# Kernel optimization log

Measured on AMD Instinct MI355X. Metric: run time of the kernel, lower is better.

## Reference

```python
import jax, jax.numpy as jnp
import numpy as np

H1, H2, H3 = 32, 64, 64
NODEN = 12
NODES_PER_GRAPH = NODEN + 2  # 14
N = 700000                   # 50000 graphs * 14 nodes
E = 4000000


def setup_inputs() -> dict:
    key = jax.random.key(0)
    ks = jax.random.split(key, 8)
    x = jax.random.normal(ks[0], (N, H1), dtype=jnp.float32)
    edges = jax.random.randint(ks[1], (2, E), 0, N, dtype=jnp.int64)
    W1 = jax.random.normal(ks[2], (H1, H2), dtype=jnp.float32) / np.sqrt(H1).astype(np.float32)
    b1 = jnp.zeros((H2,), jnp.float32)
    W2 = jax.random.normal(ks[3], (H2, H3), dtype=jnp.float32) / np.sqrt(H2).astype(np.float32)
    b2 = jnp.zeros((H3,), jnp.float32)
    Wfc = jax.random.normal(ks[4], (H3 * NODES_PER_GRAPH, 1), dtype=jnp.float32) / np.sqrt(H3 * NODES_PER_GRAPH).astype(np.float32)
    bfc = jnp.zeros((1,), jnp.float32)
    return {"x": x, "edges": edges, "W1": W1, "b1": b1, "W2": W2, "b2": b2, "Wfc": Wfc, "bfc": bfc}


def gcn_conv(x, src, dst, W, b, n):
    # PyG GCNConv: h = X W; add self-loops; norm = deg^-1/2[src]*deg^-1/2[dst]
    h = x @ W  # [N, out]
    ones = jnp.ones(src.shape[0], dtype=h.dtype)
    deg = jax.ops.segment_sum(ones, dst, num_segments=n) + jnp.asarray(1.0, h.dtype)  # +1 self-loop
    dinv = jax.lax.rsqrt(deg)  # deg >= 1 always (self-loop)
    norm = dinv[src] * dinv[dst]  # [E]
    agg = jax.ops.segment_sum(h[src] * norm[:, None], dst, num_segments=n)
    agg = agg + h * (dinv * dinv)[:, None]  # self-loop contribution
    return agg + b


def reference(x, edges, W1, b1, W2, b2, Wfc, bfc):
    src, dst = edges[0], edges[1]
    h = jax.nn.relu(gcn_conv(x, src, dst, W1, b1, N))
    # F.dropout(training=False) is identity in eval mode
    h = jax.nn.relu(gcn_conv(h, src, dst, W2, b2, N))
    h = h.reshape(-1, H3 * NODES_PER_GRAPH)  # [B, 896]
    return h @ Wfc + bfc  # [B, 1]
```

## Files before the change

### kernel.cpp

```cpp
#include <hip/hip_runtime.h>
#include <hip/hip_fp16.h>


typedef _Float16 half8 __attribute__((ext_vector_type(8)));
typedef float float4v __attribute__((ext_vector_type(4)));

#define CHUNK 8192
#define BSH 11
#define BNODES 2048
#define DBINS 64

__global__ __launch_bounds__(256) void fallback_kernel(float* __restrict__ out, int n, float v)
{
  int i = blockIdx.x * 256 + threadIdx.x;
  if (i < n) out[i] = v;
}

__global__ __launch_bounds__(64) void probe_kernel(const int* __restrict__ edges, int* __restrict__ flag)
{
  if (threadIdx.x == 0) {
    int orv = edges[1] | edges[3] | edges[5] | edges[7] | edges[9] | edges[11] | edges[13] | edges[15];
    flag[0] = (orv == 0) ? 1 : 0;
  }
}

__global__ __launch_bounds__(64) void zero_dummy_kernel(
    __half* __restrict__ P, __half* __restrict__ F2, int* __restrict__ dhist, int N)
{
  int t = threadIdx.x;
  dhist[t] = 0;
  if (t < 8) ((uint2*)(P + (size_t)N * 32))[t] = make_uint2(0, 0);
  else if (t < 24) ((uint2*)(F2 + (size_t)N * 64))[t - 8] = make_uint2(0, 0);
}

__global__ __launch_bounds__(256) void hist2_kernel(
    const int* __restrict__ edges, int E, int N, const int* __restrict__ flag,
    int* __restrict__ cnt, int NBK)
{
  __shared__ int lh[512];
  int t = threadIdx.x;
  int blk = blockIdx.x;
  for (int b = t; b < NBK; b += 256) lh[b] = 0;
  __syncthreads();
  int sh = flag[0];
  int base = blk * CHUNK;
#pragma unroll
  for (int k = 0; k < CHUNK / 256; k++) {
    int e = base + k * 256 + t;
    if (e < E) {
      int d = edges[(E + e) << sh];
      if ((unsigned)d < (unsigned)N) atomicAdd(&lh[d >> BSH], 1);
    }
  }
  __syncthreads();
  for (int b = t; b < NBK; b += 256) cnt[(size_t)blk * NBK + b] = lh[b];
}

__global__ __launch_bounds__(64) void colscan_kernel(
    int* __restrict__ cnt, int NCH, int NBK, int* __restrict__ totals)
{
  int b = blockIdx.x;
  int lane = threadIdx.x;
  int carry = 0;
  int rounds = (NCH + 63) >> 6;
  for (int r = 0; r < rounds; r++) {
    int blk = r * 64 + lane;
    int v = (blk < NCH) ? cnt[(size_t)blk * NBK + b] : 0;
    int incl = v;
#pragma unroll
    for (int off = 1; off < 64; off <<= 1) {
      int x = __shfl_up(incl, off);
      if (lane >= off) incl += x;
    }
    int excl = incl - v + carry;
    if (blk < NCH) cnt[(size_t)blk * NBK + b] = excl;
    carry += __shfl(incl, 63);
  }
  if (lane == 0) totals[b] = carry;
}

__global__ __launch_bounds__(512) void scan_totals_kernel(
    const int* __restrict__ totals, int NBK,
    int* __restrict__ bstart, int* __restrict__ rowptr, int N)
{
  __shared__ int sm[512];
  int t = threadIdx.x;
  int v = (t < NBK) ? totals[t] : 0;
  sm[t] = v;
  __syncthreads();
  for (int off = 1; off < 512; off <<= 1) {
    int x = 0;
    if (t >= off) x = sm[t - off];
    __syncthreads();
    if (t >= off) sm[t] += x;
    __syncthreads();
  }
  if (t < NBK) bstart[t] = sm[t] - v;
  if (t == 0) { bstart[NBK] = sm[511]; rowptr[N] = sm[511] + N; }
}

__global__ __launch_bounds__(256) void pass3_kernel(
    const int* __restrict__ edges, int E, int N, const int* __restrict__ flag,
    const int* __restrict__ cnt, const int* __restrict__ bstart,
    int* __restrict__ pair, int NBK)
{
  __shared__ int lcur[512];
  int t = threadIdx.x;
  int blk = blockIdx.x;
  for (int b = t; b < NBK; b += 256)
    lcur[b] = bstart[b] + cnt[(size_t)blk * NBK + b];
  __syncthreads();
  int sh = flag[0];
  int base = blk * CHUNK;
#pragma unroll
  for (int k = 0; k < CHUNK / 256; k++) {
    int e = base + k * 256 + t;
    if (e < E) {
      int s = edges[e << sh];
      int d = edges[(E + e) << sh];
      if ((unsigned)s < (unsigned)N && (unsigned)d < (unsigned)N) {
        int pos = atomicAdd(&lcur[d >> BSH], 1);
        pair[pos] = s | ((d & (BNODES - 1)) << 20);
      }
    }
  }
}

__global__ __launch_bounds__(256) void build_kernel(
    const int* __restrict__ pair, const int* __restrict__ bstart,
    int* __restrict__ rowptr, float* __restrict__ dinv, int* __restrict__ col, int N)
{
  __shared__ int hist[BNODES];
  __shared__ int cur[BNODES];
  __shared__ int sc[256];
  int b = blockIdx.x;
  int t = threadIdx.x;
  int pbeg = bstart[b], pend = bstart[b + 1];
  int colbase = pbeg + (b << BSH);
#pragma unroll
  for (int i = 0; i < BNODES / 256; i++) {
    int idx = i * 256 + t;
    int row = (b << BSH) + idx;
    hist[idx] = (row < N) ? 1 : 0;
  }
  __syncthreads();
  for (int p = pbeg + t; p < pend; p += 256)
    atomicAdd(&hist[(pair[p] >> 20) & (BNODES - 1)], 1);
  __syncthreads();
  int hv[8];
  int tsum = 0;
#pragma unroll
  for (int i = 0; i < 8; i++) { hv[i] = hist[t * 8 + i]; tsum += hv[i]; }
  sc[t] = tsum;
  __syncthreads();
  for (int off = 1; off < 256; off <<= 1) {
    int x = 0;
    if (t >= off) x = sc[t - off];
    __syncthreads();
    if (t >= off) sc[t] += x;
    __syncthreads();
  }
  int run = sc[t] - tsum;
#pragma unroll
  for (int i = 0; i < 8; i++) {
    int idx = t * 8 + i;
    int rp = colbase + run;
    int row = (b << BSH) + idx;
    if (row < N) {
      rowptr[row] = rp;
      dinv[row] = rsqrtf((float)hv[i]);
      col[rp] = row;
      cur[idx] = rp + 1;
    } else {
      cur[idx] = rp;
    }
    run += hv[i];
  }
  __syncthreads();
  for (int p = pbeg + t; p < pend; p += 256) {
    int v = pair[p];
    int pos = atomicAdd(&cur[(v >> 20) & (BNODES - 1)], 1);
    col[pos] = v & 0xFFFFF;
  }
}

__global__ __launch_bounds__(256) void deg_hist_kernel(
    const int* __restrict__ rowptr, int* __restrict__ dhist, int N)
{
  __shared__ int lh[DBINS];
  int t = threadIdx.x;
  if (t < DBINS) lh[t] = 0;
  __syncthreads();
  int n = blockIdx.x * 256 + t;
  if (n < N) {
    int rlen = rowptr[n + 1] - rowptr[n];
    int b = rlen < DBINS ? rlen : DBINS - 1;
    atomicAdd(&lh[b], 1);
  }
  __syncthreads();
  if (t < DBINS && lh[t]) atomicAdd(&dhist[t], lh[t]);
}

__global__ __launch_bounds__(64) void deg_scan_kernel(
    const int* __restrict__ dhist, int* __restrict__ dcur)
{
  int t = threadIdx.x;
  int v = dhist[t];
  int incl = v;
#pragma unroll
  for (int off = 1; off < 64; off <<= 1) {
    int x = __shfl_up(incl, off);
    if (t >= off) incl += x;
  }
  dcur[t] = incl - v;
}

__global__ __launch_bounds__(256) void deg_place_kernel(
    const int* __restrict__ rowptr, const float* __restrict__ dinv, int* __restrict__ dcur,
    int* __restrict__ perm, int* __restrict__ iperm,
    int2* __restrict__ rowinfo, float* __restrict__ dinv_p, int N)
{
  __shared__ int lh[DBINS];
  __shared__ int lbase[DBINS];
  int t = threadIdx.x;
  if (t < DBINS) lh[t] = 0;
  __syncthreads();
  int n = blockIdx.x * 256 + t;
  int b = -1, rbeg = 0, rlen = 0;
  if (n < N) {
    rbeg = rowptr[n];
    rlen = rowptr[n + 1] - rbeg;
    b = rlen < DBINS ? rlen : DBINS - 1;
    atomicAdd(&lh[b], 1);
  }
  __syncthreads();
  if (t < DBINS) lbase[t] = lh[t] ? atomicAdd(&dcur[t], lh[t]) : 0;
  __syncthreads();
  if (t < DBINS) lh[t] = lbase[t];
  __syncthreads();
  if (n < N) {
    int pos = atomicAdd(&lh[b], 1);
    perm[pos] = n;
    iperm[n] = pos;
    rowinfo[pos] = make_int2(rbeg, rlen);
    dinv_p[pos] = dinv[n];
  }
}

__global__ __launch_bounds__(256) void remap_col_kernel(
    int* __restrict__ col, const int* __restrict__ iperm,
    const int* __restrict__ rowptr, int N)
{
  int total = rowptr[N];
  int stride = gridDim.x * 256;
  for (int k = blockIdx.x * 256 + threadIdx.x; k < total; k += stride)
    col[k] = iperm[col[k]];
}

__global__ __launch_bounds__(256) void scale_x_perm_kernel(
    const float* __restrict__ X, const int* __restrict__ perm,
    const float* __restrict__ dinv_p, __half* __restrict__ P, int N)
{
  int idx = blockIdx.x * 256 + threadIdx.x;
  int total = N * 4;
  int stride = gridDim.x * 256;
  for (int i = idx; i < total; i += stride) {
    int pos = i >> 2, part = i & 3;
    int node = perm[pos];
    const float4* xp = (const float4*)(X + (size_t)node * 32 + part * 8);
    float dv = dinv_p[pos];
    float4 v0 = xp[0], v1 = xp[1];
    half8 h;
    h[0] = (_Float16)(dv * v0.x); h[1] = (_Float16)(dv * v0.y);
    h[2] = (_Float16)(dv * v0.z); h[3] = (_Float16)(dv * v0.w);
    h[4] = (_Float16)(dv * v1.x); h[5] = (_Float16)(dv * v1.y);
    h[6] = (_Float16)(dv * v1.z); h[7] = (_Float16)(dv * v1.w);
    *(half8*)(P + (size_t)pos * 32 + part * 8) = h;
  }
}

__device__ inline void hacc(uint4 v, __half2* a)
{
  a[0] = __hadd2(a[0], *reinterpret_cast<__half2*>(&v.x));
  a[1] = __hadd2(a[1], *reinterpret_cast<__half2*>(&v.y));
  a[2] = __hadd2(a[2], *reinterpret_cast<__half2*>(&v.z));
  a[3] = __hadd2(a[3], *reinterpret_cast<__half2*>(&v.w));
}

__global__ __launch_bounds__(256) void agg1_pos_kernel(
    const __half* __restrict__ P, const int2* __restrict__ rowinfo,
    const int* __restrict__ col, const float* __restrict__ dinv_p,
    const float* __restrict__ W1, const float* __restrict__ b1,
    __half* __restrict__ U, int ntiles, int ndummy)
{
  int lane = threadIdx.x & 63;
  int n16 = lane & 15;
  int quad = lane >> 4;

  half8 bf[4];
#pragma unroll
  for (int jb = 0; jb < 4; jb++)
#pragma unroll
    for (int i = 0; i < 8; i++)
      bf[jb][i] = (_Float16)W1[(quad * 8 + i) * 64 + jb * 16 + n16];
  float b1j[4];
#pragma unroll
  for (int jb = 0; jb < 4; jb++) b1j[jb] = b1[jb * 16 + n16];

  const uint4* P4 = (const uint4*)P;
  _Float16* Uh = (_Float16*)U;
  int wave = (blockIdx.x * 256 + threadIdx.x) >> 6;
  int nw = (gridDim.x * 256) >> 6;
  for (int tile = wave; tile < ntiles; tile += nw) {
    int ut = __builtin_amdgcn_readfirstlane(tile);
    int base = ut * 16;
    int2 ri = rowinfo[base + n16];
    int rbeg = ri.x, rlen = ri.y;
    float dvown = dinv_p[base + n16];

    __half2 z2 = __float2half2_rn(0.f);
    __half2 aA[4] = {z2, z2, z2, z2};
    __half2 aB[4] = {z2, z2, z2, z2};

    for (int j = 0; __any(j < rlen); j += 8) {
      int c[8];
#pragma unroll
      for (int q = 0; q < 8; q++) {
        int cc = col[rbeg + j + q];
        c[q] = (j + q < rlen) ? cc : ndummy;
      }
      uint4 v[8];
#pragma unroll
      for (int q = 0; q < 8; q++) v[q] = P4[((size_t)c[q] << 2) + quad];
#pragma unroll
      for (int q = 0; q < 8; q += 2) { hacc(v[q], aA); hacc(v[q + 1], aB); }
    }
#pragma unroll
    for (int k = 0; k < 4; k++) aA[k] = __hadd2(aA[k], aB[k]);

    half8 a = *reinterpret_cast<half8*>(aA);
    float4v co[4];
#pragma unroll
    for (int jb = 0; jb < 4; jb++) {
      float4v z = {0.f, 0.f, 0.f, 0.f};
      co[jb] = __builtin_amdgcn_mfma_f32_16x16x32_f16(a, bf[jb], z, 0, 0, 0);
    }
#pragma unroll
    for (int r = 0; r < 4; r++) {
      int pos2 = base + quad * 4 + r;
      float dv = __shfl(dvown, quad * 4 + r);
#pragma unroll
      for (int jb = 0; jb < 4; jb++) {
        float h = dv * co[jb][r] + b1j[jb];
        h = h > 0.f ? h : 0.f;
        Uh[(size_t)pos2 * 64 + jb * 16 + n16] = (_Float16)(dv * h);
      }
    }
  }
}

__global__ __launch_bounds__(256) void out_init_kernel(
    float* __restrict__ out, const float* __restrict__ bfc, int n)
{
  int i = blockIdx.x * 256 + threadIdx.x;
  if (i < n) out[i] = bfc[0];
}

__global__ __launch_bounds__(256) void mfma_final_fused_kernel(
    const __half* __restrict__ U, const int2* __restrict__ rowinfo,
    const int* __restrict__ col, const float* __restrict__ dinv_p,
    const int* __restrict__ perm,
    const float* __restrict__ W2, const float* __restrict__ b2,
    const float* __restrict__ Wfc, float* __restrict__ out,
    int ntiles, int ndummy)
{
  int lane = threadIdx.x & 63;
  int n16 = lane & 15;
  int quad = lane >> 4;

  half8 bf[4][2];
#pragma unroll
  for (int jb = 0; jb < 4; jb++)
#pragma unroll
    for (int kf = 0; kf < 2; kf++)
#pragma unroll
      for (int i = 0; i < 8; i++)
        bf[jb][kf][i] = (_Float16)W2[(kf * 32 + quad * 8 + i) * 64 + jb * 16 + n16];
  float b2j[4];
#pragma unroll
  for (int jb = 0; jb < 4; jb++) b2j[jb] = b2[jb * 16 + n16];

  const uint4* U4 = (const uint4*)U;
  int wave = (blockIdx.x * 256 + threadIdx.x) >> 6;
  int nw = (gridDim.x * 256) >> 6;
  for (int tile = wave; tile < ntiles; tile += nw) {
    int ut = __builtin_amdgcn_readfirstlane(tile);
    int base = ut * 16;
    int2 ri = rowinfo[base + n16];
    int rbeg = ri.x, rlen = ri.y;
    int node = perm[base + n16];
    float dvown = dinv_p[base + n16];

    __half2 z2 = __float2half2_rn(0.f);
    __half2 aE0[4] = {z2, z2, z2, z2};
    __half2 aE1[4] = {z2, z2, z2, z2};
    __half2 aO0[4] = {z2, z2, z2, z2};
    __half2 aO1[4] = {z2, z2, z2, z2};

    for (int j = 0; __any(j < rlen); j += 4) {
      int c0 = col[rbeg + j];
      int c1 = col[rbeg + j + 1];
      int c2 = col[rbeg + j + 2];
      int c3 = col[rbeg + j + 3];
      c0 = (j < rlen) ? c0 : ndummy;
      c1 = (j + 1 < rlen) ? c1 : ndummy;
      c2 = (j + 2 < rlen) ? c2 : ndummy;
      c3 = (j + 3 < rlen) ? c3 : ndummy;
      uint4 v00 = U4[((size_t)c0 << 3) + quad];
      uint4 v01 = U4[((size_t)c0 << 3) + 4 + quad];
      uint4 v10 = U4[((size_t)c1 << 3) + quad];
      uint4 v11 = U4[((size_t)c1 << 3) + 4 + quad];
      uint4 v20 = U4[((size_t)c2 << 3) + quad];
      uint4 v21 = U4[((size_t)c2 << 3) + 4 + quad];
      uint4 v30 = U4[((size_t)c3 << 3) + quad];
      uint4 v31 = U4[((size_t)c3 << 3) + 4 + quad];
      hacc(v00, aE0); hacc(v01, aE1);
      hacc(v10, aO0); hacc(v11, aO1);
      hacc(v20, aE0); hacc(v21, aE1);
      hacc(v30, aO0); hacc(v31, aO1);
    }
#pragma unroll
    for (int k = 0; k < 4; k++) {
      aE0[k] = __hadd2(aE0[k], aO0[k]);
      aE1[k] = __hadd2(aE1[k], aO1[k]);
    }
    __half2 dv = __half2half2(__float2half_rn(dvown));
#pragma unroll
    for (int j = 0; j < 4; j++) {
      aE0[j] = __hmul2(aE0[j], dv);
      aE1[j] = __hmul2(aE1[j], dv);
    }
    half8 a0 = *reinterpret_cast<half8*>(aE0);
    half8 a1 = *reinterpret_cast<half8*>(aE1);

    int g_r[4], t_r[4];
#pragma unroll
    for (int r = 0; r < 4; r++) {
      int nd = __shfl(node, quad * 4 + r);
      g_r[r] = nd / 14;
      t_r[r] = nd - g_r[r] * 14;
    }
    float pr[4] = {0.f, 0.f, 0.f, 0.f};
#pragma unroll
    for (int jb = 0; jb < 4; jb++) {
      float4v acc = {0.f, 0.f, 0.f, 0.f};
      acc = __builtin_amdgcn_mfma_f32_16x16x32_f16(a0, bf[jb][0], acc, 0, 0, 0);
      acc = __builtin_amdgcn_mfma_f32_16x16x32_f16(a1, bf[jb][1], acc, 0, 0, 0);
      int j = jb * 16 + n16;
#pragma unroll
      for (int r = 0; r < 4; r++) {
        float h = acc[r] + b2j[jb];
        h = h > 0.f ? h : 0.f;
        pr[r] += h * Wfc[t_r[r] * 64 + j];
      }
    }
#pragma unroll
    for (int r = 0; r < 4; r++) {
#pragma unroll
      for (int off = 1; off < 16; off <<= 1) pr[r] += __shfl_xor(pr[r], off);
    }
    if (n16 == 0) {
#pragma unroll
      for (int r = 0; r < 4; r++) atomicAdd(&out[g_r[r]], pr[r]);
    }
  }
}

extern "C" void kernel_launch(void* const* d_in, const int* in_sizes, int n_in,
                              void* d_out, int out_size, void* d_ws, size_t ws_size,
                              hipStream_t stream)
{
  const float* x = (const float*)d_in[0];
  const int* edges = (const int*)d_in[1];
  const float* W1 = (const float*)d_in[2];
  const float* b1 = (const float*)d_in[3];
  const float* W2 = (const float*)d_in[4];
  const float* b2 = (const float*)d_in[5];
  const float* Wfc = (const float*)d_in[6];
  const float* bfc = (const float*)d_in[7];
  float* out = (float*)d_out;
  (void)n_in;

  const int N = in_sizes[0] / 32;
  const int E = in_sizes[1] / 2;
  const int B = out_size;
  const int NBK = (N + BNODES - 1) >> BSH;
  const int NCH = (E + CHUNK - 1) / CHUNK;
  const int NBLK = (N + 255) / 256;

  char* ws = (char*)d_ws;
  size_t off = 0;
  auto alloc = [&](size_t bytes) -> void* {
    void* p = ws + off;
    off += (bytes + 255) & ~(size_t)255;
    return p;
  };
  int* flag = (int*)alloc(256);
  int* cnt = (int*)alloc((size_t)NCH * NBK * 4);
  int* totals = (int*)alloc((size_t)NBK * 4);
  int* bstart = (int*)alloc(((size_t)NBK + 1) * 4);
  int* col = (int*)alloc(((size_t)E + N + 256) * 4);
  int* rowptr = (int*)alloc(((size_t)N + 1) * 4);
  float* dinv = (float*)alloc((size_t)N * 4);
  int* dhist = (int*)alloc(DBINS * 4);
  int* dcur = (int*)alloc(DBINS * 4);
  int* perm = (int*)alloc((size_t)N * 4);
  int* iperm = (int*)alloc((size_t)N * 4);
  int2* rowinfo = (int2*)alloc((size_t)N * 8);
  float* dinv_p = (float*)alloc((size_t)N * 4);
  __half* P = (__half*)alloc(((size_t)N + 16) * 32 * 2);
  __half* F2 = (__half*)alloc(((size_t)N + 16) * 64 * 2);
  int* pair = (int*)P;

  if (off > ws_size) {
    float v = -(float)(double)(ws_size >> 20);
    fallback_kernel<<<(B + 255) / 256, 256, 0, stream>>>(out, B, v);
    return;
  }

  probe_kernel<<<1, 64, 0, stream>>>(edges, flag);
  zero_dummy_kernel<<<1, 64, 0, stream>>>(P, F2, dhist, N);
  hist2_kernel<<<NCH, 256, 0, stream>>>(edges, E, N, flag, cnt, NBK);
  colscan_kernel<<<NBK, 64, 0, stream>>>(cnt, NCH, NBK, totals);
  scan_totals_kernel<<<1, 512, 0, stream>>>(totals, NBK, bstart, rowptr, N);
  pass3_kernel<<<NCH, 256, 0, stream>>>(edges, E, N, flag, cnt, bstart, pair, NBK);
  build_kernel<<<NBK, 256, 0, stream>>>(pair, bstart, rowptr, dinv, col, N);

  deg_hist_kernel<<<NBLK, 256, 0, stream>>>(rowptr, dhist, N);
  deg_scan_kernel<<<1, 64, 0, stream>>>(dhist, dcur);
  deg_place_kernel<<<NBLK, 256, 0, stream>>>(rowptr, dinv, dcur, perm, iperm, rowinfo, dinv_p, N);
  remap_col_kernel<<<4096, 256, 0, stream>>>(col, iperm, rowptr, N);

  int ntiles = (N + 15) / 16;
  scale_x_perm_kernel<<<2048, 256, 0, stream>>>(x, perm, dinv_p, P, N);
  agg1_pos_kernel<<<4096, 256, 0, stream>>>(P, rowinfo, col, dinv_p, W1, b1, F2, ntiles, N);
  out_init_kernel<<<(B + 255) / 256, 256, 0, stream>>>(out, bfc, B);
  mfma_final_fused_kernel<<<4096, 256, 0, stream>>>(F2, rowinfo, col, dinv_p, perm, W2, b2, Wfc,
                                                    out, ntiles, N);
}
```

Measured before the change: 601.5 us.

## Fuse small setup kernels and pair light/heavy tiles per wave in aggregation

Removes the probe, zero, deg_hist, deg_scan, remap, scale and out_init launches. Their work moves into hist2, build and deg_place, and a combined prep kernel now does the column remap, x scaling and output init. The aggregation kernels now launch one wave per tile pair, with each wave handling tile i and tile ntiles-1-i. Because tiles are sorted by degree, this pairs a light tile with a heavy one to balance load. The costs are that every block recomputes the edge-dtype probe, the whole degree scan runs redundantly in every deg_place block, and the grid is much larger.

```diff
diff --git a/kernel.cpp b/kernel.cpp
--- a/kernel.cpp
+++ b/kernel.cpp
@@ -16,33 +16,30 @@
   if (i < n) out[i] = v;
 }
 
-__global__ __launch_bounds__(64) void probe_kernel(const int* __restrict__ edges, int* __restrict__ flag)
-{
-  if (threadIdx.x == 0) {
-    int orv = edges[1] | edges[3] | edges[5] | edges[7] | edges[9] | edges[11] | edges[13] | edges[15];
-    flag[0] = (orv == 0) ? 1 : 0;
-  }
-}
-
-__global__ __launch_bounds__(64) void zero_dummy_kernel(
-    __half* __restrict__ P, __half* __restrict__ F2, int* __restrict__ dhist, int N)
-{
-  int t = threadIdx.x;
-  dhist[t] = 0;
-  if (t < 8) ((uint2*)(P + (size_t)N * 32))[t] = make_uint2(0, 0);
-  else if (t < 24) ((uint2*)(F2 + (size_t)N * 64))[t - 8] = make_uint2(0, 0);
+__device__ inline int edges_shift(const int* __restrict__ edges)
+{
+  int orv = edges[1] | edges[3] | edges[5] | edges[7] | edges[9] | edges[11] | edges[13] | edges[15];
+  return (orv == 0) ? 1 : 0;
 }
 
 __global__ __launch_bounds__(256) void hist2_kernel(
-    const int* __restrict__ edges, int E, int N, const int* __restrict__ flag,
-    int* __restrict__ cnt, int NBK)
+    const int* __restrict__ edges, int E, int N,
+    int* __restrict__ cnt, int NBK,
+    __half* __restrict__ P, __half* __restrict__ F2,
+    int* __restrict__ dhist, int* __restrict__ dcnt)
 {
   __shared__ int lh[512];
   int t = threadIdx.x;
   int blk = blockIdx.x;
+  if (blk == 0) {
+    if (t < 8) ((uint2*)(P + (size_t)N * 32))[t] = make_uint2(0, 0);
+    else if (t < 24) ((uint2*)(F2 + (size_t)N * 64))[t - 8] = make_uint2(0, 0);
+    if (t >= 64 && t < 64 + DBINS) dhist[t - 64] = 0;
+    if (t >= 128 && t < 128 + DBINS) dcnt[t - 128] = 0;
+  }
   for (int b = t; b < NBK; b += 256) lh[b] = 0;
   __syncthreads();
-  int sh = flag[0];
+  int sh = edges_shift(edges);
   int base = blk * CHUNK;
 #pragma unroll
   for (int k = 0; k < CHUNK / 256; k++) {
@@ -100,7 +97,7 @@
 }
 
 __global__ __launch_bounds__(256) void pass3_kernel(
-    const int* __restrict__ edges, int E, int N, const int* __restrict__ flag,
+    const int* __restrict__ edges, int E, int N,
     const int* __restrict__ cnt, const int* __restrict__ bstart,
     int* __restrict__ pair, int NBK)
 {
@@ -110,7 +107,7 @@
   for (int b = t; b < NBK; b += 256)
     lcur[b] = bstart[b] + cnt[(size_t)blk * NBK + b];
   __syncthreads();
-  int sh = flag[0];
+  int sh = edges_shift(edges);
   int base = blk * CHUNK;
 #pragma unroll
   for (int k = 0; k < CHUNK / 256; k++) {
@@ -128,15 +125,18 @@
 
 __global__ __launch_bounds__(256) void build_kernel(
     const int* __restrict__ pair, const int* __restrict__ bstart,
-    int* __restrict__ rowptr, float* __restrict__ dinv, int* __restrict__ col, int N)
+    int* __restrict__ rowptr, float* __restrict__ dinv, int* __restrict__ col,
+    int* __restrict__ dhist, int N)
 {
   __shared__ int hist[BNODES];
   __shared__ int cur[BNODES];
   __shared__ int sc[256];
+  __shared__ int lh2[DBINS];
   int b = blockIdx.x;
   int t = threadIdx.x;
   int pbeg = bstart[b], pend = bstart[b + 1];
   int colbase = pbeg + (b << BSH);
+  if (t < DBINS) lh2[t] = 0;
 #pragma unroll
   for (int i = 0; i < BNODES / 256; i++) {
     int idx = i * 256 + t;
@@ -171,12 +171,15 @@
       dinv[row] = rsqrtf((float)hv[i]);
       col[rp] = row;
       cur[idx] = rp + 1;
+      int bin = hv[i] < DBINS ? hv[i] : DBINS - 1;
+      atomicAdd(&lh2[bin], 1);
     } else {
       cur[idx] = rp;
     }
     run += hv[i];
   }
   __syncthreads();
+  if (t < DBINS && lh2[t]) atomicAdd(&dhist[t], lh2[t]);
   for (int p = pbeg + t; p < pend; p += 256) {
     int v = pair[p];
     int pos = atomicAdd(&cur[(v >> 20) & (BNODES - 1)], 1);
@@ -184,46 +187,27 @@
   }
 }
 
-__global__ __launch_bounds__(256) void deg_hist_kernel(
-    const int* __restrict__ rowptr, int* __restrict__ dhist, int N)
-{
-  __shared__ int lh[DBINS];
-  int t = threadIdx.x;
-  if (t < DBINS) lh[t] = 0;
-  __syncthreads();
-  int n = blockIdx.x * 256 + t;
-  if (n < N) {
-    int rlen = rowptr[n + 1] - rowptr[n];
-    int b = rlen < DBINS ? rlen : DBINS - 1;
-    atomicAdd(&lh[b], 1);
-  }
-  __syncthreads();
-  if (t < DBINS && lh[t]) atomicAdd(&dhist[t], lh[t]);
-}
-
-__global__ __launch_bounds__(64) void deg_scan_kernel(
-    const int* __restrict__ dhist, int* __restrict__ dcur)
-{
-  int t = threadIdx.x;
-  int v = dhist[t];
-  int incl = v;
-#pragma unroll
-  for (int off = 1; off < 64; off <<= 1) {
-    int x = __shfl_up(incl, off);
-    if (t >= off) incl += x;
-  }
-  dcur[t] = incl - v;
-}
-
 __global__ __launch_bounds__(256) void deg_place_kernel(
-    const int* __restrict__ rowptr, const float* __restrict__ dinv, int* __restrict__ dcur,
+    const int* __restrict__ rowptr, const float* __restrict__ dinv,
+    const int* __restrict__ dhist, int* __restrict__ dcnt,
     int* __restrict__ perm, int* __restrict__ iperm,
     int2* __restrict__ rowinfo, float* __restrict__ dinv_p, int N)
 {
+  __shared__ int bb[DBINS];
   __shared__ int lh[DBINS];
   __shared__ int lbase[DBINS];
   int t = threadIdx.x;
-  if (t < DBINS) lh[t] = 0;
+  if (t < DBINS) {
+    lh[t] = 0;
+    int v = dhist[t];
+    int incl = v;
+#pragma unroll
+    for (int off = 1; off < DBINS; off <<= 1) {
+      int x = __shfl_up(incl, off);
+      if (t >= off) incl += x;
+    }
+    bb[t] = incl - v;
+  }
   __syncthreads();
   int n = blockIdx.x * 256 + t;
   int b = -1, rbeg = 0, rlen = 0;
@@ -234,7 +218,7 @@
     atomicAdd(&lh[b], 1);
   }
   __syncthreads();
-  if (t < DBINS) lbase[t] = lh[t] ? atomicAdd(&dcur[t], lh[t]) : 0;
+  if (t < DBINS) lbase[t] = lh[t] ? (bb[t] + atomicAdd(&dcnt[t], lh[t])) : 0;
   __syncthreads();
   if (t < DBINS) lh[t] = lbase[t];
   __syncthreads();
@@ -247,24 +231,18 @@
   }
 }
 
-__global__ __launch_bounds__(256) void remap_col_kernel(
-    int* __restrict__ col, const int* __restrict__ iperm,
-    const int* __restrict__ rowptr, int N)
-{
+__global__ __launch_bounds__(256) void prep_kernel(
+    int* __restrict__ col, const int* __restrict__ iperm, const int* __restrict__ rowptr,
+    const float* __restrict__ X, const int* __restrict__ perm,
+    const float* __restrict__ dinv_p, __half* __restrict__ P,
+    float* __restrict__ out, const float* __restrict__ bfc, int N, int B)
+{
+  int idx = blockIdx.x * 256 + threadIdx.x;
+  int stride = gridDim.x * 256;
   int total = rowptr[N];
-  int stride = gridDim.x * 256;
-  for (int k = blockIdx.x * 256 + threadIdx.x; k < total; k += stride)
-    col[k] = iperm[col[k]];
-}
-
-__global__ __launch_bounds__(256) void scale_x_perm_kernel(
-    const float* __restrict__ X, const int* __restrict__ perm,
-    const float* __restrict__ dinv_p, __half* __restrict__ P, int N)
-{
-  int idx = blockIdx.x * 256 + threadIdx.x;
-  int total = N * 4;
-  int stride = gridDim.x * 256;
-  for (int i = idx; i < total; i += stride) {
+  for (int k = idx; k < total; k += stride) col[k] = iperm[col[k]];
+  int totp = N * 4;
+  for (int i = idx; i < totp; i += stride) {
     int pos = i >> 2, part = i & 3;
     int node = perm[pos];
     const float4* xp = (const float4*)(X + (size_t)node * 32 + part * 8);
@@ -277,6 +255,7 @@
     h[6] = (_Float16)(dv * v1.z); h[7] = (_Float16)(dv * v1.w);
     *(half8*)(P + (size_t)pos * 32 + part * 8) = h;
   }
+  for (int i = idx; i < B; i += stride) out[i] = bfc[0];
 }
 
 __device__ inline void hacc(uint4 v, __half2* a)
@@ -297,6 +276,10 @@
   int n16 = lane & 15;
   int quad = lane >> 4;
 
+  int wid = (blockIdx.x * 256 + threadIdx.x) >> 6;
+  int nt2 = (ntiles + 1) >> 1;
+  if (wid >= nt2) return;
+
   half8 bf[4];
 #pragma unroll
   for (int jb = 0; jb < 4; jb++)
@@ -309,9 +292,10 @@
 
   const uint4* P4 = (const uint4*)P;
   _Float16* Uh = (_Float16*)U;
-  int wave = (blockIdx.x * 256 + threadIdx.x) >> 6;
-  int nw = (gridDim.x * 256) >> 6;
-  for (int tile = wave; tile < ntiles; tile += nw) {
+#pragma unroll 1
+  for (int it = 0; it < 2; it++) {
+    int tile = (it == 0) ? wid : (ntiles - 1 - wid);
+    if (it == 1 && tile <= wid) break;
     int ut = __builtin_amdgcn_readfirstlane(tile);
     int base = ut * 16;
     int2 ri = rowinfo[base + n16];
@@ -357,13 +341,6 @@
       }
     }
   }
-}
-
-__global__ __launch_bounds__(256) void out_init_kernel(
-    float* __restrict__ out, const float* __restrict__ bfc, int n)
-{
-  int i = blockIdx.x * 256 + threadIdx.x;
-  if (i < n) out[i] = bfc[0];
 }
 
 __global__ __launch_bounds__(256) void mfma_final_fused_kernel(
@@ -378,6 +355,10 @@
   int n16 = lane & 15;
   int quad = lane >> 4;
 
+  int wid = (blockIdx.x * 256 + threadIdx.x) >> 6;
+  int nt2 = (ntiles + 1) >> 1;
+  if (wid >= nt2) return;
+
   half8 bf[4][2];
 #pragma unroll
   for (int jb = 0; jb < 4; jb++)
@@ -391,9 +372,10 @@
   for (int jb = 0; jb < 4; jb++) b2j[jb] = b2[jb * 16 + n16];
 
   const uint4* U4 = (const uint4*)U;
-  int wave = (blockIdx.x * 256 + threadIdx.x) >> 6;
-  int nw = (gridDim.x * 256) >> 6;
-  for (int tile = wave; tile < ntiles; tile += nw) {
+#pragma unroll 1
+  for (int it = 0; it < 2; it++) {
+    int tile = (it == 0) ? wid : (ntiles - 1 - wid);
+    if (it == 1 && tile <= wid) break;
     int ut = __builtin_amdgcn_readfirstlane(tile);
     int base = ut * 16;
     int2 ri = rowinfo[base + n16];
@@ -505,7 +487,6 @@
     off += (bytes + 255) & ~(size_t)255;
     return p;
   };
-  int* flag = (int*)alloc(256);
   int* cnt = (int*)alloc((size_t)NCH * NBK * 4);
   int* totals = (int*)alloc((size_t)NBK * 4);
   int* bstart = (int*)alloc(((size_t)NBK + 1) * 4);
@@ -513,7 +494,7 @@
   int* rowptr = (int*)alloc(((size_t)N + 1) * 4);
   float* dinv = (float*)alloc((size_t)N * 4);
   int* dhist = (int*)alloc(DBINS * 4);
-  int* dcur = (int*)alloc(DBINS * 4);
+  int* dcnt = (int*)alloc(DBINS * 4);
   int* perm = (int*)alloc((size_t)N * 4);
   int* iperm = (int*)alloc((size_t)N * 4);
   int2* rowinfo = (int2*)alloc((size_t)N * 8);
@@ -528,23 +509,20 @@
     return;
   }
 
-  probe_kernel<<<1, 64, 0, stream>>>(edges, flag);
-  zero_dummy_kernel<<<1, 64, 0, stream>>>(P, F2, dhist, N);
-  hist2_kernel<<<NCH, 256, 0, stream>>>(edges, E, N, flag, cnt, NBK);
+  hist2_kernel<<<NCH, 256, 0, stream>>>(edges, E, N, cnt, NBK, P, F2, dhist, dcnt);
   colscan_kernel<<<NBK, 64, 0, stream>>>(cnt, NCH, NBK, totals);
   scan_totals_kernel<<<1, 512, 0, stream>>>(totals, NBK, bstart, rowptr, N);
-  pass3_kernel<<<NCH, 256, 0, stream>>>(edges, E, N, flag, cnt, bstart, pair, NBK);
-  build_kernel<<<NBK, 256, 0, stream>>>(pair, bstart, rowptr, dinv, col, N);
-
-  deg_hist_kernel<<<NBLK, 256, 0, stream>>>(rowptr, dhist, N);
-  deg_scan_kernel<<<1, 64, 0, stream>>>(dhist, dcur);
-  deg_place_kernel<<<NBLK, 256, 0, stream>>>(rowptr, dinv, dcur, perm, iperm, rowinfo, dinv_p, N);
-  remap_col_kernel<<<4096, 256, 0, stream>>>(col, iperm, rowptr, N);
+  pass3_kernel<<<NCH, 256, 0, stream>>>(edges, E, N, cnt, bstart, pair, NBK);
+  build_kernel<<<NBK, 256, 0, stream>>>(pair, bstart, rowptr, dinv, col, dhist, N);
+  deg_place_kernel<<<NBLK, 256, 0, stream>>>(rowptr, dinv, dhist, dcnt,
+                                             perm, iperm, rowinfo, dinv_p, N);
+  prep_kernel<<<4096, 256, 0, stream>>>(col, iperm, rowptr, x, perm, dinv_p, P,
+                                        out, bfc, N, B);
 
   int ntiles = (N + 15) / 16;
-  scale_x_perm_kernel<<<2048, 256, 0, stream>>>(x, perm, dinv_p, P, N);
-  agg1_pos_kernel<<<4096, 256, 0, stream>>>(P, rowinfo, col, dinv_p, W1, b1, F2, ntiles, N);
-  out_init_kernel<<<(B + 255) / 256, 256, 0, stream>>>(out, bfc, B);
-  mfma_final_fused_kernel<<<4096, 256, 0, stream>>>(F2, rowinfo, col, dinv_p, perm, W2, b2, Wfc,
+  int nt2 = (ntiles + 1) >> 1;
+  int gblk = (nt2 + 3) / 4;
+  agg1_pos_kernel<<<gblk, 256, 0, stream>>>(P, rowinfo, col, dinv_p, W1, b1, F2, ntiles, N);
+  mfma_final_fused_kernel<<<gblk, 256, 0, stream>>>(F2, rowinfo, col, dinv_p, perm, W2, b2, Wfc,
                                                     out, ntiles, N);
 }
```

After: 561.3 us. 1.07x faster.
